# Kernel optimization log

Measured on AMD Instinct MI355X. Metric: run time of the kernel, lower is better.

The kernel has to match this reference:

```python
import jax, jax.numpy as jnp
import numpy as np
import math

CH_IN, MID, PS, DSTATE = 64, 128, 1024, 16
DTRANK = math.ceil(PS / 16)  # 64
B, H, W = 4, 256, 256


def conv2d(x, w, b=None, stride=1, pad=0, groups=1):
    out = jax.lax.conv_general_dilated(
        x, w, (stride, stride), [(pad, pad), (pad, pad)],
        feature_group_count=groups, dimension_numbers=('NCHW', 'OIHW', 'NCHW'))
    return out if b is None else out + b[None, :, None, None]


def groupnorm(x, g, b, ngroups=2, eps=1e-5):
    bb, c, hh, ww = x.shape
    xr = x.reshape(bb, ngroups, c // ngroups, hh, ww)
    mu = xr.mean(axis=(2, 3, 4), keepdims=True)
    var = xr.var(axis=(2, 3, 4), keepdims=True)
    xn = ((xr - mu) * jax.lax.rsqrt(var + eps)).reshape(bb, c, hh, ww)
    return xn * g[None, :, None, None] + b[None, :, None, None]


def silu(x):
    return x * jax.nn.sigmoid(x)


def selective_scan(u, delta, A, Bm, Cm, D):
    # u, delta: (b, l, d); A: (d, n); Bm, Cm: (b, l, n); D: (d,)
    dA = jnp.exp(jnp.einsum('bld,dn->bldn', delta, A))          # (b,l,d,n)
    dBu = (delta * u)[..., None] * Bm[:, :, None, :]             # (b,l,d,n)
    bsz, l, d = u.shape
    n = A.shape[1]

    def step(carry, inp):
        dA_i, dBu_i, C_i = inp                                   # (b,d,n),(b,d,n),(b,n)
        carry = dA_i * carry + dBu_i
        y = jnp.einsum('bdn,bn->bd', carry, C_i)
        return carry, y

    x0 = jnp.zeros((bsz, d, n), dtype=u.dtype)
    _, ys = jax.lax.scan(step, x0, (dA.transpose(1, 0, 2, 3), dBu.transpose(1, 0, 2, 3), Cm.transpose(1, 0, 2)))
    y = ys.transpose(1, 0, 2)                                    # (b,l,d)
    return y + u * D


def mamba_block(x, inproj_w, conv_w, conv_b, xproj_w, dtp_w, dtp_b, alog, dd):
    xr = conv2d(x, inproj_w, None, 1, 1, MID // 2)               # (b, 2*MID, h, w)
    xs, res = jnp.split(xr, 2, axis=1)
    xs = silu(conv2d(xs, conv_w, conv_b, 1, 0, MID // 2))
    b, c, h, w = xs.shape
    u = xs.reshape(b, c, h * w)                                  # (b, l=c, d=h*w)
    A = -jnp.exp(alog.astype(jnp.float32))                       # (d, n)
    x_dbl = jnp.einsum('bld,kd->blk', u, xproj_w)
    delta, Bm, Cm = jnp.split(x_dbl, [DTRANK, DTRANK + DSTATE], axis=-1)
    delta = jax.nn.softplus(jnp.einsum('blr,dr->bld', delta, dtp_w) + dtp_b)
    y = selective_scan(u, delta, A, Bm, Cm, dd.astype(jnp.float32))
    y = y.reshape(b, c, h, w)
    return y * silu(res)


def forward(x, w_in, b_in,
            gn0_g, gn0_b, inproj0_w, conv0_w, conv0_b, xproj0_w, dtp0_w, dtp0_b, alog0, dd0,
            gn1_g, gn1_b, inproj1_w, conv1_w, conv1_b, xproj1_w, dtp1_w, dtp1_b, alog1, dd1,
            w_out, b_out):
    h = conv2d(x, w_in, b_in, 8, 0, CH_IN // 2)                  # (B, MID, H/8, W/8)
    h = mamba_block(groupnorm(h, gn0_g, gn0_b), inproj0_w, conv0_w, conv0_b, xproj0_w, dtp0_w, dtp0_b, alog0, dd0) + h
    h = mamba_block(groupnorm(h, gn1_g, gn1_b), inproj1_w, conv1_w, conv1_b, xproj1_w, dtp1_w, dtp1_b, alog1, dd1) + h
    out = conv2d(h, w_out, b_out, 1, 0, CH_IN // 2)
    out = jax.image.resize(out, (out.shape[0], out.shape[1], out.shape[2] * 8, out.shape[3] * 8), method='bilinear')
    return out


def setup_inputs():
    key = jax.random.key(0)
    ks = jax.random.split(key, 16)
    def rn(k, shp, s=0.05):
        return s * jax.random.normal(k, shp, jnp.float32)
    alog = jnp.log(jnp.broadcast_to(jnp.arange(1, DSTATE + 1, dtype=jnp.float32), (PS, DSTATE)))
    inp = {
        'x': jax.random.normal(ks[0], (B, CH_IN, H, W), jnp.float32),
        'w_in': rn(ks[1], (MID, 2, 8, 8)), 'b_in': jnp.zeros((MID,), jnp.float32),
        'gn0_g': jnp.ones((MID,), jnp.float32), 'gn0_b': jnp.zeros((MID,), jnp.float32),
        'inproj0_w': rn(ks[2], (2 * MID, 2, 3, 3)),
        'conv0_w': rn(ks[3], (MID, 2, 1, 1)), 'conv0_b': jnp.zeros((MID,), jnp.float32),
        'xproj0_w': rn(ks[4], (DTRANK + 2 * DSTATE, PS), 0.02),
        'dtp0_w': rn(ks[5], (PS, DTRANK), 0.02), 'dtp0_b': rn(ks[6], (PS,), 0.02),
        'alog0': alog, 'dd0': jnp.ones((PS,), jnp.float32),
        'gn1_g': jnp.ones((MID,), jnp.float32), 'gn1_b': jnp.zeros((MID,), jnp.float32),
        'inproj1_w': rn(ks[7], (2 * MID, 2, 3, 3)),
        'conv1_w': rn(ks[8], (MID, 2, 1, 1)), 'conv1_b': jnp.zeros((MID,), jnp.float32),
        'xproj1_w': rn(ks[9], (DTRANK + 2 * DSTATE, PS), 0.02),
        'dtp1_w': rn(ks[10], (PS, DTRANK), 0.02), 'dtp1_b': rn(ks[11], (PS,), 0.02),
        'alog1': alog, 'dd1': jnp.ones((PS,), jnp.float32),
        'w_out': rn(ks[12], (MID, MID // (CH_IN // 2), 1, 1)), 'b_out': jnp.zeros((MID,), jnp.float32),
    }
    return inp


def reference(x, w_in, b_in,
              gn0_g, gn0_b, inproj0_w, conv0_w, conv0_b, xproj0_w, dtp0_w, dtp0_b, alog0, dd0,
              gn1_g, gn1_b, inproj1_w, conv1_w, conv1_b, xproj1_w, dtp1_w, dtp1_b, alog1, dd1,
              w_out, b_out):
    return forward(x, w_in, b_in,
                   gn0_g, gn0_b, inproj0_w, conv0_w, conv0_b, xproj0_w, dtp0_w, dtp0_b, alog0, dd0,
                   gn1_g, gn1_b, inproj1_w, conv1_w, conv1_b, xproj1_w, dtp1_w, dtp1_b, alog1, dd1,
                   w_out, b_out)
```

## Files before the change

kernel.cpp:

```cpp
#include <hip/hip_runtime.h>
#include <hip/hip_bf16.h>

#define BN 4
#define MID 128
#define P 1024
#define PS 1024
#define DSTATE 16
#define DTRANK 64
#define XD 96
#define HOUT 256

typedef __hip_bfloat16 bf16;

__device__ __forceinline__ float b2f(bf16 v) { return __bfloat162float(v); }
__device__ __forceinline__ float dload(const void* p, int i, bool isbf) {
  return isbf ? b2f(((const bf16*)p)[i]) : ((const float*)p)[i];
}
__device__ __forceinline__ float bfl(unsigned u) {
  union { unsigned i; float f; } c; c.i = u << 16; return c.f;
}
__device__ __forceinline__ float bfh(unsigned u) {
  union { unsigned i; float f; } c; c.i = u & 0xffff0000u; return c.f;
}
__device__ __forceinline__ float softplusf(float a) {
  return fmaxf(a, 0.f) + log1pf(__expf(-fabsf(a)));
}

#define NPARAM 24
#define TOTAL_PARAMS 392192
#define CONV_PER_BLOCK 766
struct PtrPack { const void* p[NPARAM]; };

__device__ __forceinline__ void find_tensor(int dst, int& tt, int& off) {
  const int offs[NPARAM + 1] = {0,16384,16512,16640,16768,21376,21632,21760,120064,185600,
                                186624,203008,204032,204160,204288,208896,209152,209280,
                                307584,373120,374144,390528,391552,392064,392192};
  int t = 0, base = 0;
#pragma unroll
  for (int q = 1; q < NPARAM; ++q) {
    if (dst >= offs[q]) { t = q; base = offs[q]; }
  }
  tt = t; off = dst - base;
}

__global__ __launch_bounds__(256) void conv_in_kernel(
    const void* __restrict__ x, const unsigned* __restrict__ alog_raw,
    PtrPack pk, float* __restrict__ pp, float* __restrict__ h,
    float2* __restrict__ partA) {
  bool isbf = (alog_raw[0] != 0u);
  int blk = blockIdx.x, t = threadIdx.x;

  for (int i = t; i < CONV_PER_BLOCK; i += 256) {
    int dst = blk * CONV_PER_BLOCK + i;
    int tt, off;
    find_tensor(dst, tt, off);
    int src = off;
    if (tt == 7 || tt == 17) {
      int j = off & 3, q = off >> 2;
      int k = q % 96, d4 = q / 96;
      src = k * 1024 + d4 * 4 + j;
    } else if (tt == 8 || tt == 18) {
      src = (off & 1023) * 64 + (off >> 10);
    }
    pp[dst] = dload(pk.p[tt], src, isbf);
  }

  __shared__ float wlds[512];
  __shared__ float blds[4];
  __shared__ float ls[8];
  int tid = blk * 256 + t;
  int p = tid & 1023; int g = (tid >> 10) & 31; int b = tid >> 15;
  for (int q = t; q < 512; q += 256) {
    int i = q >> 8, kh = (q >> 5) & 7, j = (q >> 3) & 3, kw = q & 7;
    wlds[q] = dload(pk.p[0], (g * 4 + j) * 128 + i * 64 + kh * 8 + kw, isbf);
  }
  if (t < 4) blds[t] = dload(pk.p[1], g * 4 + t, isbf);
  __syncthreads();

  int oy = p >> 5, ox = p & 31;
  float acc0 = blds[0], acc1 = blds[1], acc2 = blds[2], acc3 = blds[3];
  if (isbf) {
    const uint4* xp = (const uint4*)x;
    size_t base = ((size_t)b * 64 + g * 2) * 8192;
    for (int i = 0; i < 2; ++i) {
      size_t cb = base + (size_t)i * 8192 + (size_t)oy * 256 + ox;
#pragma unroll
      for (int kh = 0; kh < 8; ++kh) {
        uint4 v = xp[cb + kh * 32];
        float xv[8] = {bfl(v.x),bfh(v.x),bfl(v.y),bfh(v.y),bfl(v.z),bfh(v.z),bfl(v.w),bfh(v.w)};
        const float* wk = &wlds[(i * 8 + kh) * 32];
#pragma unroll
        for (int kw = 0; kw < 8; ++kw) {
          float xvv = xv[kw];
          acc0 += xvv * wk[kw];
          acc1 += xvv * wk[8 + kw];
          acc2 += xvv * wk[16 + kw];
          acc3 += xvv * wk[24 + kw];
        }
      }
    }
  } else {
    const float4* xf = (const float4*)x;
    size_t base = ((size_t)b * 64 + g * 2) * 16384;
    for (int i = 0; i < 2; ++i) {
      size_t cb = base + (size_t)i * 16384 + (size_t)oy * 512 + ox * 2;
#pragma unroll
      for (int kh = 0; kh < 8; ++kh) {
        float4 v0 = xf[cb + kh * 64];
        float4 v1 = xf[cb + kh * 64 + 1];
        float xv[8] = {v0.x,v0.y,v0.z,v0.w,v1.x,v1.y,v1.z,v1.w};
        const float* wk = &wlds[(i * 8 + kh) * 32];
#pragma unroll
        for (int kw = 0; kw < 8; ++kw) {
          float xvv = xv[kw];
          acc0 += xvv * wk[kw];
          acc1 += xvv * wk[8 + kw];
          acc2 += xvv * wk[16 + kw];
          acc3 += xvv * wk[24 + kw];
        }
      }
    }
  }
  size_t ob = ((size_t)b * 128 + g * 4) * 1024 + p;
  h[ob] = acc0; h[ob + 1024] = acc1; h[ob + 2048] = acc2; h[ob + 3072] = acc3;

  float s  = acc0 + acc1 + acc2 + acc3;
  float s2 = acc0*acc0 + acc1*acc1 + acc2*acc2 + acc3*acc3;
#pragma unroll
  for (int off = 32; off > 0; off >>= 1) { s += __shfl_xor(s, off); s2 += __shfl_xor(s2, off); }
  int wid = t >> 6;
  if ((t & 63) == 0) { ls[wid * 2] = s; ls[wid * 2 + 1] = s2; }
  __syncthreads();
  if (t == 0)
    partA[blk] = make_float2(ls[0] + ls[2] + ls[4] + ls[6],
                             ls[1] + ls[3] + ls[5] + ls[7]);
}

__global__ __launch_bounds__(256) void fuse_u_xdbl_kernel(
    const float* __restrict__ hin, const float2* __restrict__ part, int poff, int pstride,
    const float* __restrict__ gng, const float* __restrict__ gnb,
    const float* __restrict__ iw, const float* __restrict__ cw, const float* __restrict__ cb,
    const float* __restrict__ xwp, const float* __restrict__ dwt, const float* __restrict__ db,
    float* __restrict__ u_t, float* __restrict__ dlt_t, float* __restrict__ bct) {
  int bid = blockIdx.x;
  int s = bid & 1, g3 = (bid >> 1) & 31, b = bid >> 6;
  int t = threadIdx.x;
  int ic0 = g3 * 2;
  __shared__ float tile[2][34][36];
  __shared__ float4 us4[4][256];
  __shared__ float4 accs4[96];
  __shared__ float xds[4][64];
  __shared__ float sred[2];

  if (t < 64) {
    float2 v = part[b * 128 + poff + t * pstride];
    float ss = v.x, s2 = v.y;
#pragma unroll
    for (int off = 32; off > 0; off >>= 1) { ss += __shfl_xor(ss, off); s2 += __shfl_xor(s2, off); }
    if (t == 0) { sred[0] = ss; sred[1] = s2; }
  }
  for (int q = t; q < 2448; q += 256) ((float*)tile)[q] = 0.f;
  __syncthreads();
  float mu = sred[0] * (1.f / 65536.f);
  float var = sred[1] * (1.f / 65536.f) - mu * mu;
  float rs = rsqrtf(var + 1e-5f);
  float a0 = rs * gng[ic0],     o0 = gnb[ic0]     - mu * a0;
  float a1 = rs * gng[ic0 + 1], o1 = gnb[ic0 + 1] - mu * a1;
  const float* h0 = hin + ((size_t)b * MID + ic0) * P;
  for (int q = t; q < 2048; q += 256) {
    int ch = q >> 10, px = q & 1023, y = px >> 5, xx = px & 31;
    float v = h0[ch * P + px];
    tile[ch][y + 1][xx + 1] = ch ? (v * a1 + o1) : (v * a0 + o0);
  }
  __syncthreads();

  const float* w0 = iw + (size_t)(4 * g3) * 18;
  float* usf = (float*)us4;
#pragma unroll
  for (int q = 0; q < 4; ++q) {
    int px = q * 256 + t;
    int y = px >> 5, xx = px & 31;
    float nb0[9], nb1[9];
#pragma unroll
    for (int ky = 0; ky < 3; ++ky)
#pragma unroll
      for (int kx = 0; kx < 3; ++kx) {
        nb0[ky * 3 + kx] = tile[0][y + ky][xx + kx];
        nb1[ky * 3 + kx] = tile[1][y + ky][xx + kx];
      }
    float xsv[4];
#pragma unroll
    for (int s4 = 0; s4 < 4; ++s4) {
      const float* wr = w0 + s4 * 18;
      float acc = 0.f;
#pragma unroll
      for (int k = 0; k < 9; ++k) acc += nb0[k] * wr[k] + nb1[k] * wr[9 + k];
      xsv[s4] = acc;
    }
#pragma unroll
    for (int j = 0; j < 4; ++j) {
      int c = 4 * g3 + j;
      int e4 = (j >> 1) * 2;
      float acc = cb[c] + cw[2 * c] * xsv[e4] + cw[2 * c + 1] * xsv[e4 + 1];
      usf[j * 1024 + px] = acc / (1.f + __expf(-acc));
    }
  }
  __syncthreads();

  float a0_ = 0.f, a1_ = 0.f, a2_ = 0.f, a3_ = 0.f;
  if (t < 192) {
    int kh = (t >= 96) ? 1 : 0, k = t - 96 * kh;
    const float4* wp = (const float4*)xwp;
#pragma unroll 4
    for (int i = 0; i < 128; ++i) {
      int d4 = 2 * i + kh;
      float4 w4 = wp[d4 * 96 + k];
      float4 u0 = us4[0][d4], u1 = us4[1][d4], u2 = us4[2][d4], u3 = us4[3][d4];
      a0_ += u0.x * w4.x + u0.y * w4.y + u0.z * w4.z + u0.w * w4.w;
      a1_ += u1.x * w4.x + u1.y * w4.y + u1.z * w4.z + u1.w * w4.w;
      a2_ += u2.x * w4.x + u2.y * w4.y + u2.z * w4.z + u2.w * w4.w;
      a3_ += u3.x * w4.x + u3.y * w4.y + u3.z * w4.z + u3.w * w4.w;
    }
    if (kh) accs4[k] = make_float4(a0_, a1_, a2_, a3_);
  } else if (s == 0) {
    for (int i = t - 192; i < 1024; i += 64) {
      float4 uv = make_float4(usf[i], usf[1024 + i], usf[2048 + i], usf[3072 + i]);
      *(float4*)(u_t + ((size_t)b * 1024 + i) * 128 + 4 * g3) = uv;
    }
  }
  __syncthreads();
  if (t < 96) {
    float4 o = accs4[t];
    float v0 = a0_ + o.x, v1 = a1_ + o.y, v2 = a2_ + o.z, v3 = a3_ + o.w;
    if (t < 64) {
      xds[0][t] = v0; xds[1][t] = v1; xds[2][t] = v2; xds[3][t] = v3;
    } else if (s == 0) {
      *(float4*)(bct + ((size_t)b * 32 + (t - 64)) * 128 + 4 * g3) = make_float4(v0, v1, v2, v3);
    }
  }
  __syncthreads();

  int d0 = 512 * s + t, d1 = d0 + 256;
  float bias0 = db[d0], bias1 = db[d1];
  float acc00 = bias0, acc01 = bias0, acc02 = bias0, acc03 = bias0;
  float acc10 = bias1, acc11 = bias1, acc12 = bias1, acc13 = bias1;
#pragma unroll 8
  for (int r = 0; r < 64; ++r) {
    float x0 = xds[0][r], x1 = xds[1][r], x2 = xds[2][r], x3 = xds[3][r];
    const float* wr = dwt + r * 1024 + 512 * s + t;
    float w0_ = wr[0], w1_ = wr[256];
    acc00 += x0 * w0_; acc01 += x1 * w0_; acc02 += x2 * w0_; acc03 += x3 * w0_;
    acc10 += x0 * w1_; acc11 += x1 * w1_; acc12 += x2 * w1_; acc13 += x3 * w1_;
  }
  *(float4*)(dlt_t + ((size_t)b * 1024 + d0) * 128 + 4 * g3) =
      make_float4(softplusf(acc00), softplusf(acc01), softplusf(acc02), softplusf(acc03));
  *(float4*)(dlt_t + ((size_t)b * 1024 + d1) * 128 + 4 * g3) =
      make_float4(softplusf(acc10), softplusf(acc11), softplusf(acc12), softplusf(acc13));
}

__global__ __launch_bounds__(256) void scan_merge_kernel(
    const float* __restrict__ hin, const float2* __restrict__ part, int poff, int pstride,
    const float* __restrict__ gng, const float* __restrict__ gnb, const float* __restrict__ iw,
    const float* __restrict__ u_t, const float* __restrict__ dlt_t, const float* __restrict__ bct,
    const float* __restrict__ alog, const float* __restrict__ dd_,
    float* __restrict__ hout, float2* __restrict__ part_out) {
  int bid = blockIdx.x;
  int q = bid & 63, b = bid >> 6;
  int t = threadIdx.x;
  int n = t & 15, dl = t >> 4;
  int d = q * 16 + dl;
  __shared__ float y_s[16][132];
  __shared__ float hs[64][3][18];
  __shared__ float a_s[64], o_s[64];
  __shared__ float sred[2];
  __shared__ float ls[8];

  if (t < 64) {
    float2 v = part[b * 128 + poff + t * pstride];
    float ss = v.x, s2 = v.y;
#pragma unroll
    for (int off = 32; off > 0; off >>= 1) { ss += __shfl_xor(ss, off); s2 += __shfl_xor(s2, off); }
    if (t == 0) { sred[0] = ss; sred[1] = s2; }
  }
  __syncthreads();
  float mu = sred[0] * (1.f / 65536.f);
  float var = sred[1] * (1.f / 65536.f) - mu * mu;
  float rs = rsqrtf(var + 1e-5f);
  if (t < 64) {
    float aa = rs * gng[64 + t];
    a_s[t] = aa;
    o_s[t] = gnb[64 + t] - mu * aa;
  }

  float A = -__expf(alog[d * DSTATE + n]);
  float D = dd_[d];
  const float4* ut = (const float4*)(u_t   + ((size_t)b * 1024 + d) * 128);
  const float4* dt = (const float4*)(dlt_t + ((size_t)b * 1024 + d) * 128);
  const float4* Bt = (const float4*)(bct + ((size_t)b * 32 + n) * 128);
  const float4* Ct = (const float4*)(bct + ((size_t)b * 32 + 16 + n) * 128);
  float state = 0.f;
#pragma unroll 2
  for (int lc = 0; lc < 32; ++lc) {
    float4 dl4 = dt[lc], u4 = ut[lc], B4 = Bt[lc], C4 = Ct[lc];
    float4 yo;
#define SSTEP(c) { float dA = __expf(dl4.c * A); state = dA * state + dl4.c * u4.c * B4.c; \
    float yv = state * C4.c; yv += __shfl_xor(yv, 1, 16); yv += __shfl_xor(yv, 2, 16); \
    yv += __shfl_xor(yv, 4, 16); yv += __shfl_xor(yv, 8, 16); yo.c = yv + u4.c * D; }
    SSTEP(x) SSTEP(y) SSTEP(z) SSTEP(w)
#undef SSTEP
    if (n == 0) *(float4*)&y_s[dl][4 * lc] = yo;
  }
  __syncthreads();

  int py = q >> 1, px0 = (q & 1) * 16;
  for (int m = t; m < 3456; m += 256) {
    int ch = m / 54, rem = m - ch * 54;
    int rr = rem / 18, cc = rem - rr * 18;
    int gy = py - 1 + rr, gx = px0 - 1 + cc;
    float v = 0.f;
    if ((unsigned)gy < 32u && (unsigned)gx < 32u)
      v = a_s[ch] * hin[((size_t)b * 128 + 64 + ch) * 1024 + gy * 32 + gx] + o_s[ch];
    hs[ch][rr][cc] = v;
  }
  __syncthreads();

  int px = t & 15, cg = t >> 4;
  int gx_ = px0 + px;
  float sacc = 0.f, s2acc = 0.f;
#pragma unroll
  for (int j = 0; j < 8; ++j) {
    int c = cg * 8 + j;
    int gq = c >> 2;
    const float* wr = iw + (size_t)(4 * (32 + gq) + (c & 3)) * 18;
    int ci = 2 * gq;
    float res = 0.f;
#pragma unroll
    for (int ky = 0; ky < 3; ++ky)
#pragma unroll
      for (int kx = 0; kx < 3; ++kx)
        res += hs[ci][ky][px + kx] * wr[ky * 3 + kx] + hs[ci + 1][ky][px + kx] * wr[9 + ky * 3 + kx];
    float sl = res / (1.f + __expf(-res));
    size_t oi = ((size_t)b * 128 + c) * 1024 + py * 32 + gx_;
    float val = y_s[px][c] * sl + hin[oi];
    hout[oi] = val;
    sacc += val; s2acc += val * val;
  }
  if (part_out) {
#pragma unroll
    for (int off = 32; off > 0; off >>= 1) { sacc += __shfl_xor(sacc, off); s2acc += __shfl_xor(s2acc, off); }
    int wid = t >> 6;
    if ((t & 63) == 0) { ls[wid * 2] = sacc; ls[wid * 2 + 1] = s2acc; }
    __syncthreads();
    if (t == 0) {
      part_out[bid * 2]     = make_float2(ls[0] + ls[2], ls[1] + ls[3]);
      part_out[bid * 2 + 1] = make_float2(ls[4] + ls[6], ls[5] + ls[7]);
    }
  }
}

__global__ __launch_bounds__(256) void out_kernel(
    const float* __restrict__ h, const float* __restrict__ w, const float* __restrict__ bias,
    const unsigned* __restrict__ alog_raw, void* __restrict__ out) {
  int bc = blockIdx.x;
  int c = bc & 127, b = bc >> 7;
  int t = threadIdx.x;
  __shared__ float cop[1024];
  __shared__ float txs[256];
  __shared__ int x0s[256], x1s[256];
  {
    float cx = ((float)t + 0.5f) * 0.125f - 0.5f;
    int ix0 = (int)floorf(cx);
    txs[t] = cx - (float)ix0;
    x0s[t] = max(ix0, 0);
    x1s[t] = min(ix0 + 1, 31);
  }
  const float* hp = h + ((size_t)b * MID + (c & ~3)) * P;
  float w0 = w[c * 4], w1 = w[c * 4 + 1], w2 = w[c * 4 + 2], w3 = w[c * 4 + 3];
  float bo = bias[c];
  {
    const float4* h4 = (const float4*)hp;
    float4 v0 = h4[t], v1 = h4[256 + t], v2 = h4[512 + t], v3 = h4[768 + t];
    float4 a;
    a.x = bo + w0 * v0.x + w1 * v1.x + w2 * v2.x + w3 * v3.x;
    a.y = bo + w0 * v0.y + w1 * v1.y + w2 * v2.y + w3 * v3.y;
    a.z = bo + w0 * v0.z + w1 * v1.z + w2 * v2.z + w3 * v3.z;
    a.w = bo + w0 * v0.w + w1 * v1.w + w2 * v2.w + w3 * v3.w;
    ((float4*)cop)[t] = a;
  }
  __syncthreads();
  bool isbf = (alog_raw[0] != 0u);
  size_t obase = (size_t)bc * 16384;
  for (int gidx = t; gidx < 16384; gidx += 256) {
    int ox4 = gidx & 63, oy = gidx >> 6;
    float ty = txs[oy]; int y0 = x0s[oy], y1 = x1s[oy];
    const float* r0 = cop + y0 * 32;
    const float* r1 = cop + y1 * 32;
    float v[4];
#pragma unroll
    for (int j = 0; j < 4; ++j) {
      int ox = ox4 * 4 + j;
      float tx = txs[ox]; int xx0 = x0s[ox], xx1 = x1s[ox];
      float v00 = r0[xx0], v01 = r0[xx1], v10 = r1[xx0], v11 = r1[xx1];
      v[j] = (1.f - ty) * ((1.f - tx) * v00 + tx * v01) + ty * ((1.f - tx) * v10 + tx * v11);
    }
    if (isbf) {
      ushort4 s;
      s.x = __hip_bfloat16_raw(__float2bfloat16(v[0])).x;
      s.y = __hip_bfloat16_raw(__float2bfloat16(v[1])).x;
      s.z = __hip_bfloat16_raw(__float2bfloat16(v[2])).x;
      s.w = __hip_bfloat16_raw(__float2bfloat16(v[3])).x;
      ((ushort4*)out)[obase + gidx] = s;
    } else {
      ((float4*)out)[obase + gidx] = make_float4(v[0], v[1], v[2], v[3]);
    }
  }
}

extern "C" void kernel_launch(void* const* d_in, const int* in_sizes, int n_in,
                              void* d_out, int out_size, void* d_ws, size_t ws_size,
                              hipStream_t stream) {
  const void* x = d_in[0];
  const unsigned* alog_raw = (const unsigned*)d_in[11];

  PtrPack pk;
  for (int i = 0; i < NPARAM; ++i) pk.p[i] = d_in[i + 1];

  float* ws = (float*)d_ws;
  float* pp    = ws;
  float* h0    = pp + TOTAL_PARAMS;
  float* h1    = h0 + 524288;
  float* u_t   = h1 + 524288;
  float* dlt_t = u_t + 524288;
  float* bct   = dlt_t + 524288;
  float* partA = bct + 16384;
  float* partB = partA + 1024;

  const float* w_out = pp + 391552;
  const float* b_out = pp + 392064;

  conv_in_kernel<<<512, 256, 0, stream>>>(x, alog_raw, pk, pp, h0, (float2*)partA);

  float* hbuf[2] = { h0, h1 };
  for (int blk = 0; blk < 2; ++blk) {
    const float* base = pp + 16512 + (size_t)blk * 187520;
    const float* gng = base, *gnb = base + 128, *iw = base + 256;
    const float* cw = base + 4864, *cb = base + 5120;
    const float* xwp = base + 5248, *dwt = base + 103552, *db = base + 169088;
    const float* alog = base + 170112, *dd = base + 186496;
    float* hin  = hbuf[blk & 1];
    float* hout = hbuf[(blk + 1) & 1];
    const float2* pIn = (const float2*)(blk ? partB : partA);
    int pstr = blk ? 2 : 1;
    int poffU = 0;
    int poffM = blk ? 1 : 64;

    fuse_u_xdbl_kernel<<<256, 256, 0, stream>>>(hin, pIn, poffU, pstr, gng, gnb,
                                                iw, cw, cb, xwp, dwt, db,
                                                u_t, dlt_t, bct);
    scan_merge_kernel<<<256, 256, 0, stream>>>(hin, pIn, poffM, pstr, gng, gnb, iw,
                                               u_t, dlt_t, bct, alog, dd, hout,
                                               blk == 0 ? (float2*)partB : nullptr);
  }

  out_kernel<<<512, 256, 0, stream>>>(h0, w_out, b_out, alog_raw, d_out);
}
```

Measured before the change: 362.3 us.

## Split work across more threads and overlap scan with halo loading

fuse_u_xdbl now runs 512 threads per block, and each block computes only its own two sequence channels (by s) rather than four with duplicated work across the s-pair. scan_merge also goes to 512 threads: half run the selective scan while the other half load the halo tile and groupnorm stats at the same time, and the merge conv caches neighbourhoods across channels. out_kernel is split into twice as many blocks, each covering half the upsampled output. The aim is to remove redundant compute and expose more parallelism on a small 256-block grid, at the cost of higher per-block register and sync pressure.

```diff
diff --git a/kernel.cpp b/kernel.cpp
--- a/kernel.cpp
+++ b/kernel.cpp
@@ -136,7 +136,7 @@
                              ls[1] + ls[3] + ls[5] + ls[7]);
 }
 
-__global__ __launch_bounds__(256) void fuse_u_xdbl_kernel(
+__global__ __launch_bounds__(512) void fuse_u_xdbl_kernel(
     const float* __restrict__ hin, const float2* __restrict__ part, int poff, int pstride,
     const float* __restrict__ gng, const float* __restrict__ gnb,
     const float* __restrict__ iw, const float* __restrict__ cw, const float* __restrict__ cb,
@@ -146,10 +146,11 @@
   int s = bid & 1, g3 = (bid >> 1) & 31, b = bid >> 6;
   int t = threadIdx.x;
   int ic0 = g3 * 2;
+  int l0 = 4 * g3 + 2 * s;
   __shared__ float tile[2][34][36];
-  __shared__ float4 us4[4][256];
-  __shared__ float4 accs4[96];
-  __shared__ float xds[4][64];
+  __shared__ float us2[2][1024];
+  __shared__ float2 accs[3][96];
+  __shared__ float xds[2][64];
   __shared__ float sred[2];
 
   if (t < 64) {
@@ -159,7 +160,7 @@
     for (int off = 32; off > 0; off >>= 1) { ss += __shfl_xor(ss, off); s2 += __shfl_xor(s2, off); }
     if (t == 0) { sred[0] = ss; sred[1] = s2; }
   }
-  for (int q = t; q < 2448; q += 256) ((float*)tile)[q] = 0.f;
+  for (int m = t; m < 2448; m += 512) ((float*)tile)[m] = 0.f;
   __syncthreads();
   float mu = sred[0] * (1.f / 65536.f);
   float var = sred[1] * (1.f / 65536.f) - mu * mu;
@@ -167,98 +168,86 @@
   float a0 = rs * gng[ic0],     o0 = gnb[ic0]     - mu * a0;
   float a1 = rs * gng[ic0 + 1], o1 = gnb[ic0 + 1] - mu * a1;
   const float* h0 = hin + ((size_t)b * MID + ic0) * P;
-  for (int q = t; q < 2048; q += 256) {
-    int ch = q >> 10, px = q & 1023, y = px >> 5, xx = px & 31;
+  for (int m = t; m < 2048; m += 512) {
+    int ch = m >> 10, px = m & 1023, y = px >> 5, xx = px & 31;
     float v = h0[ch * P + px];
     tile[ch][y + 1][xx + 1] = ch ? (v * a1 + o1) : (v * a0 + o0);
   }
   __syncthreads();
 
-  const float* w0 = iw + (size_t)(4 * g3) * 18;
-  float* usf = (float*)us4;
-#pragma unroll
-  for (int q = 0; q < 4; ++q) {
-    int px = q * 256 + t;
-    int y = px >> 5, xx = px & 31;
-    float nb0[9], nb1[9];
-#pragma unroll
-    for (int ky = 0; ky < 3; ++ky)
-#pragma unroll
-      for (int kx = 0; kx < 3; ++kx) {
-        nb0[ky * 3 + kx] = tile[0][y + ky][xx + kx];
-        nb1[ky * 3 + kx] = tile[1][y + ky][xx + kx];
-      }
-    float xsv[4];
-#pragma unroll
-    for (int s4 = 0; s4 < 4; ++s4) {
-      const float* wr = w0 + s4 * 18;
-      float acc = 0.f;
-#pragma unroll
-      for (int k = 0; k < 9; ++k) acc += nb0[k] * wr[k] + nb1[k] * wr[9 + k];
-      xsv[s4] = acc;
-    }
-#pragma unroll
-    for (int j = 0; j < 4; ++j) {
-      int c = 4 * g3 + j;
-      int e4 = (j >> 1) * 2;
-      float acc = cb[c] + cw[2 * c] * xsv[e4] + cw[2 * c + 1] * xsv[e4 + 1];
-      usf[j * 1024 + px] = acc / (1.f + __expf(-acc));
-    }
-  }
-  __syncthreads();
-
-  float a0_ = 0.f, a1_ = 0.f, a2_ = 0.f, a3_ = 0.f;
-  if (t < 192) {
-    int kh = (t >= 96) ? 1 : 0, k = t - 96 * kh;
+  {
+    const float* wA = iw + (size_t)(4 * g3 + 2 * s) * 18;
+    const float* wB = wA + 18;
+    float cwA0 = cw[2 * l0],       cwB0 = cw[2 * l0 + 1],     cb0 = cb[l0];
+    float cwA1 = cw[2 * (l0 + 1)], cwB1 = cw[2 * (l0 + 1) + 1], cb1 = cb[l0 + 1];
+#pragma unroll
+    for (int qq = 0; qq < 2; ++qq) {
+      int px = qq * 512 + t;
+      int y = px >> 5, xx = px & 31;
+      float xsA = 0.f, xsB = 0.f;
+#pragma unroll
+      for (int ky = 0; ky < 3; ++ky)
+#pragma unroll
+        for (int kx = 0; kx < 3; ++kx) {
+          float t0 = tile[0][y + ky][xx + kx];
+          float t1 = tile[1][y + ky][xx + kx];
+          int k = ky * 3 + kx;
+          xsA += t0 * wA[k] + t1 * wA[9 + k];
+          xsB += t0 * wB[k] + t1 * wB[9 + k];
+        }
+      float u0 = cb0 + cwA0 * xsA + cwB0 * xsB;
+      float u1 = cb1 + cwA1 * xsA + cwB1 * xsB;
+      us2[0][px] = u0 / (1.f + __expf(-u0));
+      us2[1][px] = u1 / (1.f + __expf(-u1));
+    }
+  }
+  __syncthreads();
+
+  float2 acc2 = make_float2(0.f, 0.f);
+  if (t < 384) {
+    int seg = t / 96, k = t - seg * 96;
     const float4* wp = (const float4*)xwp;
 #pragma unroll 4
-    for (int i = 0; i < 128; ++i) {
-      int d4 = 2 * i + kh;
+    for (int i = 0; i < 64; ++i) {
+      int d4 = 4 * i + seg;
       float4 w4 = wp[d4 * 96 + k];
-      float4 u0 = us4[0][d4], u1 = us4[1][d4], u2 = us4[2][d4], u3 = us4[3][d4];
-      a0_ += u0.x * w4.x + u0.y * w4.y + u0.z * w4.z + u0.w * w4.w;
-      a1_ += u1.x * w4.x + u1.y * w4.y + u1.z * w4.z + u1.w * w4.w;
-      a2_ += u2.x * w4.x + u2.y * w4.y + u2.z * w4.z + u2.w * w4.w;
-      a3_ += u3.x * w4.x + u3.y * w4.y + u3.z * w4.z + u3.w * w4.w;
-    }
-    if (kh) accs4[k] = make_float4(a0_, a1_, a2_, a3_);
-  } else if (s == 0) {
-    for (int i = t - 192; i < 1024; i += 64) {
-      float4 uv = make_float4(usf[i], usf[1024 + i], usf[2048 + i], usf[3072 + i]);
-      *(float4*)(u_t + ((size_t)b * 1024 + i) * 128 + 4 * g3) = uv;
-    }
+      float4 uA = *(const float4*)&us2[0][4 * d4];
+      float4 uB = *(const float4*)&us2[1][4 * d4];
+      acc2.x += uA.x * w4.x + uA.y * w4.y + uA.z * w4.z + uA.w * w4.w;
+      acc2.y += uB.x * w4.x + uB.y * w4.y + uB.z * w4.z + uB.w * w4.w;
+    }
+    if (seg) accs[seg - 1][k] = acc2;
+  } else {
+    for (int i = t - 384; i < 1024; i += 128)
+      *(float2*)(u_t + ((size_t)b * 1024 + i) * 128 + l0) = make_float2(us2[0][i], us2[1][i]);
   }
   __syncthreads();
   if (t < 96) {
-    float4 o = accs4[t];
-    float v0 = a0_ + o.x, v1 = a1_ + o.y, v2 = a2_ + o.z, v3 = a3_ + o.w;
-    if (t < 64) {
-      xds[0][t] = v0; xds[1][t] = v1; xds[2][t] = v2; xds[3][t] = v3;
-    } else if (s == 0) {
-      *(float4*)(bct + ((size_t)b * 32 + (t - 64)) * 128 + 4 * g3) = make_float4(v0, v1, v2, v3);
-    }
-  }
-  __syncthreads();
-
-  int d0 = 512 * s + t, d1 = d0 + 256;
-  float bias0 = db[d0], bias1 = db[d1];
-  float acc00 = bias0, acc01 = bias0, acc02 = bias0, acc03 = bias0;
-  float acc10 = bias1, acc11 = bias1, acc12 = bias1, acc13 = bias1;
+    float2 r0 = accs[0][t], r1 = accs[1][t], r2 = accs[2][t];
+    float v0 = acc2.x + r0.x + r1.x + r2.x;
+    float v1 = acc2.y + r0.y + r1.y + r2.y;
+    if (t < 64) { xds[0][t] = v0; xds[1][t] = v1; }
+    else *(float2*)(bct + ((size_t)b * 32 + (t - 64)) * 128 + l0) = make_float2(v0, v1);
+  }
+  __syncthreads();
+
+  float b0 = db[t], b1 = db[t + 512];
+  float a00 = b0, a01 = b0, a10 = b1, a11 = b1;
 #pragma unroll 8
   for (int r = 0; r < 64; ++r) {
-    float x0 = xds[0][r], x1 = xds[1][r], x2 = xds[2][r], x3 = xds[3][r];
-    const float* wr = dwt + r * 1024 + 512 * s + t;
-    float w0_ = wr[0], w1_ = wr[256];
-    acc00 += x0 * w0_; acc01 += x1 * w0_; acc02 += x2 * w0_; acc03 += x3 * w0_;
-    acc10 += x0 * w1_; acc11 += x1 * w1_; acc12 += x2 * w1_; acc13 += x3 * w1_;
-  }
-  *(float4*)(dlt_t + ((size_t)b * 1024 + d0) * 128 + 4 * g3) =
-      make_float4(softplusf(acc00), softplusf(acc01), softplusf(acc02), softplusf(acc03));
-  *(float4*)(dlt_t + ((size_t)b * 1024 + d1) * 128 + 4 * g3) =
-      make_float4(softplusf(acc10), softplusf(acc11), softplusf(acc12), softplusf(acc13));
-}
-
-__global__ __launch_bounds__(256) void scan_merge_kernel(
+    float x0 = xds[0][r], x1 = xds[1][r];
+    const float* wr = dwt + r * 1024 + t;
+    float w0_ = wr[0], w1_ = wr[512];
+    a00 += x0 * w0_; a01 += x1 * w0_;
+    a10 += x0 * w1_; a11 += x1 * w1_;
+  }
+  *(float2*)(dlt_t + ((size_t)b * 1024 + t) * 128 + l0) =
+      make_float2(softplusf(a00), softplusf(a01));
+  *(float2*)(dlt_t + ((size_t)b * 1024 + t + 512) * 128 + l0) =
+      make_float2(softplusf(a10), softplusf(a11));
+}
+
+__global__ __launch_bounds__(512) void scan_merge_kernel(
     const float* __restrict__ hin, const float2* __restrict__ part, int poff, int pstride,
     const float* __restrict__ gng, const float* __restrict__ gnb, const float* __restrict__ iw,
     const float* __restrict__ u_t, const float* __restrict__ dlt_t, const float* __restrict__ bct,
@@ -267,78 +256,86 @@
   int bid = blockIdx.x;
   int q = bid & 63, b = bid >> 6;
   int t = threadIdx.x;
-  int n = t & 15, dl = t >> 4;
-  int d = q * 16 + dl;
+  int py = q >> 1, px0 = (q & 1) * 16;
   __shared__ float y_s[16][132];
   __shared__ float hs[64][3][18];
   __shared__ float a_s[64], o_s[64];
-  __shared__ float sred[2];
-  __shared__ float ls[8];
-
-  if (t < 64) {
-    float2 v = part[b * 128 + poff + t * pstride];
-    float ss = v.x, s2 = v.y;
-#pragma unroll
-    for (int off = 32; off > 0; off >>= 1) { ss += __shfl_xor(ss, off); s2 += __shfl_xor(s2, off); }
-    if (t == 0) { sred[0] = ss; sred[1] = s2; }
-  }
-  __syncthreads();
-  float mu = sred[0] * (1.f / 65536.f);
-  float var = sred[1] * (1.f / 65536.f) - mu * mu;
-  float rs = rsqrtf(var + 1e-5f);
-  if (t < 64) {
-    float aa = rs * gng[64 + t];
-    a_s[t] = aa;
-    o_s[t] = gnb[64 + t] - mu * aa;
-  }
-
-  float A = -__expf(alog[d * DSTATE + n]);
-  float D = dd_[d];
-  const float4* ut = (const float4*)(u_t   + ((size_t)b * 1024 + d) * 128);
-  const float4* dt = (const float4*)(dlt_t + ((size_t)b * 1024 + d) * 128);
-  const float4* Bt = (const float4*)(bct + ((size_t)b * 32 + n) * 128);
-  const float4* Ct = (const float4*)(bct + ((size_t)b * 32 + 16 + n) * 128);
-  float state = 0.f;
+  __shared__ float ls[16];
+
+  if (t < 256) {
+    int n = t & 15, dl = t >> 4;
+    int d = q * 16 + dl;
+    float A = -__expf(alog[d * DSTATE + n]);
+    float D = dd_[d];
+    const float4* ut = (const float4*)(u_t   + ((size_t)b * 1024 + d) * 128);
+    const float4* dt = (const float4*)(dlt_t + ((size_t)b * 1024 + d) * 128);
+    const float4* Bt = (const float4*)(bct + ((size_t)b * 32 + n) * 128);
+    const float4* Ct = (const float4*)(bct + ((size_t)b * 32 + 16 + n) * 128);
+    float state = 0.f;
 #pragma unroll 2
-  for (int lc = 0; lc < 32; ++lc) {
-    float4 dl4 = dt[lc], u4 = ut[lc], B4 = Bt[lc], C4 = Ct[lc];
-    float4 yo;
+    for (int lc = 0; lc < 32; ++lc) {
+      float4 dl4 = dt[lc], u4 = ut[lc], B4 = Bt[lc], C4 = Ct[lc];
+      float4 yo;
 #define SSTEP(c) { float dA = __expf(dl4.c * A); state = dA * state + dl4.c * u4.c * B4.c; \
-    float yv = state * C4.c; yv += __shfl_xor(yv, 1, 16); yv += __shfl_xor(yv, 2, 16); \
-    yv += __shfl_xor(yv, 4, 16); yv += __shfl_xor(yv, 8, 16); yo.c = yv + u4.c * D; }
-    SSTEP(x) SSTEP(y) SSTEP(z) SSTEP(w)
+      float yv = state * C4.c; yv += __shfl_xor(yv, 1, 16); yv += __shfl_xor(yv, 2, 16); \
+      yv += __shfl_xor(yv, 4, 16); yv += __shfl_xor(yv, 8, 16); yo.c = yv + u4.c * D; }
+      SSTEP(x) SSTEP(y) SSTEP(z) SSTEP(w)
 #undef SSTEP
-    if (n == 0) *(float4*)&y_s[dl][4 * lc] = yo;
-  }
-  __syncthreads();
-
-  int py = q >> 1, px0 = (q & 1) * 16;
-  for (int m = t; m < 3456; m += 256) {
+      if (n == 0) *(float4*)&y_s[dl][4 * lc] = yo;
+    }
+  } else {
+    int tt = t - 256;
+    if (tt < 64) {
+      float2 v = part[b * 128 + poff + tt * pstride];
+      float ss = v.x, s2 = v.y;
+#pragma unroll
+      for (int off = 32; off > 0; off >>= 1) { ss += __shfl_xor(ss, off); s2 += __shfl_xor(s2, off); }
+      float mu = ss * (1.f / 65536.f);
+      float var = s2 * (1.f / 65536.f) - mu * mu;
+      float rs = rsqrtf(var + 1e-5f);
+      float aa = rs * gng[64 + tt];
+      a_s[tt] = aa;
+      o_s[tt] = gnb[64 + tt] - mu * aa;
+    }
+    for (int m = tt; m < 3456; m += 256) {
+      int ch = m / 54, rem = m - ch * 54;
+      int rr = rem / 18, cc = rem - rr * 18;
+      int gy = py - 1 + rr, gx = px0 - 1 + cc;
+      float v = 0.f;
+      if ((unsigned)gy < 32u && (unsigned)gx < 32u)
+        v = hin[((size_t)b * 128 + 64 + ch) * 1024 + gy * 32 + gx];
+      ((float*)hs)[m] = v;
+    }
+  }
+  __syncthreads();
+  for (int m = t; m < 3456; m += 512) {
     int ch = m / 54, rem = m - ch * 54;
     int rr = rem / 18, cc = rem - rr * 18;
     int gy = py - 1 + rr, gx = px0 - 1 + cc;
-    float v = 0.f;
     if ((unsigned)gy < 32u && (unsigned)gx < 32u)
-      v = a_s[ch] * hin[((size_t)b * 128 + 64 + ch) * 1024 + gy * 32 + gx] + o_s[ch];
-    hs[ch][rr][cc] = v;
+      ((float*)hs)[m] = a_s[ch] * ((float*)hs)[m] + o_s[ch];
   }
   __syncthreads();
 
   int px = t & 15, cg = t >> 4;
+  int ci = 2 * cg;
   int gx_ = px0 + px;
+  float nbA[9], nbB[9];
+#pragma unroll
+  for (int ky = 0; ky < 3; ++ky)
+#pragma unroll
+    for (int kx = 0; kx < 3; ++kx) {
+      nbA[ky * 3 + kx] = hs[ci][ky][px + kx];
+      nbB[ky * 3 + kx] = hs[ci + 1][ky][px + kx];
+    }
   float sacc = 0.f, s2acc = 0.f;
 #pragma unroll
-  for (int j = 0; j < 8; ++j) {
-    int c = cg * 8 + j;
-    int gq = c >> 2;
-    const float* wr = iw + (size_t)(4 * (32 + gq) + (c & 3)) * 18;
-    int ci = 2 * gq;
+  for (int j = 0; j < 4; ++j) {
+    int c = 4 * cg + j;
+    const float* wr = iw + (size_t)(4 * (32 + cg) + j) * 18;
     float res = 0.f;
 #pragma unroll
-    for (int ky = 0; ky < 3; ++ky)
-#pragma unroll
-      for (int kx = 0; kx < 3; ++kx)
-        res += hs[ci][ky][px + kx] * wr[ky * 3 + kx] + hs[ci + 1][ky][px + kx] * wr[9 + ky * 3 + kx];
+    for (int k = 0; k < 9; ++k) res += nbA[k] * wr[k] + nbB[k] * wr[9 + k];
     float sl = res / (1.f + __expf(-res));
     size_t oi = ((size_t)b * 128 + c) * 1024 + py * 32 + gx_;
     float val = y_s[px][c] * sl + hin[oi];
@@ -352,8 +349,10 @@
     if ((t & 63) == 0) { ls[wid * 2] = sacc; ls[wid * 2 + 1] = s2acc; }
     __syncthreads();
     if (t == 0) {
-      part_out[bid * 2]     = make_float2(ls[0] + ls[2], ls[1] + ls[3]);
-      part_out[bid * 2 + 1] = make_float2(ls[4] + ls[6], ls[5] + ls[7]);
+      part_out[bid * 2]     = make_float2(ls[0] + ls[2] + ls[4] + ls[6],
+                                          ls[1] + ls[3] + ls[5] + ls[7]);
+      part_out[bid * 2 + 1] = make_float2(ls[8] + ls[10] + ls[12] + ls[14],
+                                          ls[9] + ls[11] + ls[13] + ls[15]);
     }
   }
 }
@@ -361,7 +360,8 @@
 __global__ __launch_bounds__(256) void out_kernel(
     const float* __restrict__ h, const float* __restrict__ w, const float* __restrict__ bias,
     const unsigned* __restrict__ alog_raw, void* __restrict__ out) {
-  int bc = blockIdx.x;
+  int bid = blockIdx.x;
+  int half = bid & 1, bc = bid >> 1;
   int c = bc & 127, b = bc >> 7;
   int t = threadIdx.x;
   __shared__ float cop[1024];
@@ -390,7 +390,8 @@
   __syncthreads();
   bool isbf = (alog_raw[0] != 0u);
   size_t obase = (size_t)bc * 16384;
-  for (int gidx = t; gidx < 16384; gidx += 256) {
+  int g0 = half * 8192;
+  for (int gidx = g0 + t; gidx < g0 + 8192; gidx += 256) {
     int ox4 = gidx & 63, oy = gidx >> 6;
     float ty = txs[oy]; int y0 = x0s[oy], y1 = x1s[oy];
     const float* r0 = cop + y0 * 32;
@@ -404,12 +405,12 @@
       v[j] = (1.f - ty) * ((1.f - tx) * v00 + tx * v01) + ty * ((1.f - tx) * v10 + tx * v11);
     }
     if (isbf) {
-      ushort4 s;
-      s.x = __hip_bfloat16_raw(__float2bfloat16(v[0])).x;
-      s.y = __hip_bfloat16_raw(__float2bfloat16(v[1])).x;
-      s.z = __hip_bfloat16_raw(__float2bfloat16(v[2])).x;
-      s.w = __hip_bfloat16_raw(__float2bfloat16(v[3])).x;
-      ((ushort4*)out)[obase + gidx] = s;
+      ushort4 sv;
+      sv.x = __hip_bfloat16_raw(__float2bfloat16(v[0])).x;
+      sv.y = __hip_bfloat16_raw(__float2bfloat16(v[1])).x;
+      sv.z = __hip_bfloat16_raw(__float2bfloat16(v[2])).x;
+      sv.w = __hip_bfloat16_raw(__float2bfloat16(v[3])).x;
+      ((ushort4*)out)[obase + gidx] = sv;
     } else {
       ((float4*)out)[obase + gidx] = make_float4(v[0], v[1], v[2], v[3]);
     }
@@ -454,13 +455,13 @@
     int poffU = 0;
     int poffM = blk ? 1 : 64;
 
-    fuse_u_xdbl_kernel<<<256, 256, 0, stream>>>(hin, pIn, poffU, pstr, gng, gnb,
+    fuse_u_xdbl_kernel<<<256, 512, 0, stream>>>(hin, pIn, poffU, pstr, gng, gnb,
                                                 iw, cw, cb, xwp, dwt, db,
                                                 u_t, dlt_t, bct);
-    scan_merge_kernel<<<256, 256, 0, stream>>>(hin, pIn, poffM, pstr, gng, gnb, iw,
+    scan_merge_kernel<<<256, 512, 0, stream>>>(hin, pIn, poffM, pstr, gng, gnb, iw,
                                                u_t, dlt_t, bct, alog, dd, hout,
                                                blk == 0 ? (float2*)partB : nullptr);
   }
 
-  out_kernel<<<512, 256, 0, stream>>>(h0, w_out, b_out, alog_raw, d_out);
-}
+  out_kernel<<<1024, 256, 0, stream>>>(h0, w_out, b_out, alog_raw, d_out);
+}
```

New measurement: 322.8 us. 10.9% less time.
